# Optimization experiments

Hardware: AMD Instinct MI355X
Metric: run time of the kernel (lower is better)

## Reference

```python
import jax, jax.numpy as jnp
import numpy as np

EPS_LOG = 1e-8
EPS_CHECK = 1e-4


def to_float8(x, exp_bits=4, mant_bits=3):
    # fp8 emulation: sign/abs/log2/floor/clamp/round chain
    max_exp = 2 ** (exp_bits - 1) - 1
    min_exp = -max_exp
    scale = 2.0 ** mant_bits
    sign = jnp.sign(x)
    x_abs = jnp.abs(x)
    exp = jnp.clip(jnp.floor(jnp.log2(x_abs + EPS_LOG)), min_exp, max_exp)
    pow2 = jnp.exp2(exp)
    mant = x_abs / pow2 - 1.0
    mant_q = jnp.round(mant * scale) / scale
    return sign * (1.0 + mant_q) * pow2


def checksum_verify(left, right, epsilon=EPS_CHECK):
    # ABFT: augment left with a column-sum row, right with a row-sum column
    left_cs = jnp.concatenate([left, jnp.sum(left, axis=0, keepdims=True)], axis=0)
    right_cs = jnp.concatenate([right, jnp.sum(right, axis=1, keepdims=True)], axis=1)
    prod_cs = left_cs @ right_cs  # [(m+1), (n+1)]
    output = prod_cs[:-1, :-1]
    row_sum_check = prod_cs[:-1, -1]
    col_sum_check = prod_cs[-1, :-1]
    col_diff = jnp.abs(jnp.sum(output, axis=0) - col_sum_check)
    row_diff = jnp.abs(jnp.sum(output, axis=1) - row_sum_check)
    mask = (row_diff > epsilon)[:, None] & (col_diff > epsilon)[None, :]
    return output, mask


def setup_inputs() -> dict:
    key = jax.random.key(0)
    kx, ku, kA, kB, kC = jax.random.split(key, 5)
    batch, n, m, p = 4096, 2048, 1024, 1024
    return {
        "x": jax.random.normal(kx, (batch, n), dtype=jnp.float32),
        "u": jax.random.normal(ku, (batch, m), dtype=jnp.float32),
        "A": jax.random.normal(kA, (n, n), dtype=jnp.float32),
        "B": jax.random.normal(kB, (n, m), dtype=jnp.float32),
        "C": jax.random.normal(kC, (p, n), dtype=jnp.float32),
    }


def reference(x, u, A, B, C):
    int_bits, frac_bits = 4, 3
    Aq = to_float8(A, int_bits, frac_bits)
    Bq = to_float8(B, int_bits, frac_bits)
    left_term, left_mask = checksum_verify(x, Aq.T)
    right_term, right_mask = checksum_verify(u, Bq.T)
    x_next = to_float8(left_term + right_term, int_bits, frac_bits)
    _ = left_mask | right_mask  # mask computed but discarded in forward (as in torch)
    Cq = to_float8(C, int_bits, frac_bits)
    y = to_float8(x_next @ Cq.T, int_bits, frac_bits)
    return (x_next, y)
```

## Files before the change

kernel.cpp:

```cpp
#include <hip/hip_runtime.h>
#include <hip/hip_bf16.h>
#include <stdint.h>

typedef __bf16 bf16_t;
typedef __attribute__((ext_vector_type(8))) __bf16 bf16x8;
typedef __attribute__((ext_vector_type(4))) float f32x4;

__device__ __forceinline__ float q8(float v) {
    float a = __builtin_fabsf(v);
    float z = a + 1e-8f;
    int ei = ((__float_as_int(z) >> 23) & 0xff) - 127;
    ei = ei > 7 ? 7 : (ei < -7 ? -7 : ei);
    float p  = __int_as_float((ei + 127) << 23);
    float ip = __int_as_float((127 - ei) << 23);
    float m  = __builtin_fmaf(a, ip, -1.0f);
    float mq = __builtin_rintf(m * 8.0f) * 0.125f;
    float r  = (1.0f + mq) * p;
    return v < 0.0f ? -r : r;
}

__device__ __forceinline__ void gload_lds16(const bf16_t* g, bf16_t* l) {
    __builtin_amdgcn_global_load_lds(
        (__attribute__((address_space(1))) void*)(g),
        (__attribute__((address_space(3))) void*)(l), 16, 0, 0);
}

__device__ __forceinline__ bf16x8 cvt8(float4 a, float4 b) {
    bf16x8 o = { (bf16_t)a.x, (bf16_t)a.y, (bf16_t)a.z, (bf16_t)a.w,
                 (bf16_t)b.x, (bf16_t)b.y, (bf16_t)b.z, (bf16_t)b.w };
    return o;
}
__device__ __forceinline__ bf16x8 q8x8(float4 a, float4 b) {
    bf16x8 o = { (bf16_t)q8(a.x), (bf16_t)q8(a.y), (bf16_t)q8(a.z), (bf16_t)q8(a.w),
                 (bf16_t)q8(b.x), (bf16_t)q8(b.y), (bf16_t)q8(b.z), (bf16_t)q8(b.w) };
    return o;
}

__global__ void pack_all(const float* __restrict__ x, const float* __restrict__ u,
                         const float* __restrict__ A, const float* __restrict__ B,
                         const float* __restrict__ C,
                         bf16_t* __restrict__ XU, bf16_t* __restrict__ AB,
                         bf16_t* __restrict__ CQ) {
    const unsigned bid = blockIdx.x;
    const int tid = threadIdx.x;
    if (bid < 4096u) {
        size_t r = bid; int col = tid * 8;
        float4 v0 = *(const float4*)&x[r * 2048 + col];
        float4 v1 = *(const float4*)&x[r * 2048 + col + 4];
        *(bf16x8*)&XU[r * 3072 + col] = cvt8(v0, v1);
    } else if (bid < 6144u) {
        unsigned b = bid - 4096u;
        size_t r = b * 2 + (tid >> 7); int col = (tid & 127) * 8;
        float4 v0 = *(const float4*)&u[r * 1024 + col];
        float4 v1 = *(const float4*)&u[r * 1024 + col + 4];
        *(bf16x8*)&XU[r * 3072 + 2048 + col] = cvt8(v0, v1);
    } else if (bid < 8192u) {
        size_t r = bid - 6144u; int col = tid * 8;
        float4 v0 = *(const float4*)&A[r * 2048 + col];
        float4 v1 = *(const float4*)&A[r * 2048 + col + 4];
        *(bf16x8*)&AB[r * 3072 + col] = q8x8(v0, v1);
    } else if (bid < 9216u) {
        unsigned b = bid - 8192u;
        size_t r = b * 2 + (tid >> 7); int col = (tid & 127) * 8;
        float4 v0 = *(const float4*)&B[r * 1024 + col];
        float4 v1 = *(const float4*)&B[r * 1024 + col + 4];
        *(bf16x8*)&AB[r * 3072 + 2048 + col] = q8x8(v0, v1);
    } else {
        size_t r = bid - 9216u; int col = tid * 8;
        float4 v0 = *(const float4*)&C[r * 2048 + col];
        float4 v1 = *(const float4*)&C[r * 2048 + col + 4];
        *(bf16x8*)&CQ[r * 2048 + col] = q8x8(v0, v1);
    }
}

template<int NBX, bool DUAL>
__global__ __launch_bounds__(512, 4)
void gemm_q8_kernel(const bf16_t* __restrict__ A, const bf16_t* __restrict__ B,
                    float* __restrict__ outf, bf16_t* __restrict__ outb,
                    int M, int N, int K) {
    constexpr int BM = 128;
    constexpr int BN = 128;
    constexpr int BK = 64;
    constexpr int PX = NBX / 2;

    __shared__ alignas(16) bf16_t sA[2][BM * BK];
    __shared__ alignas(16) bf16_t sB[2][BN * BK];

    const int tid  = threadIdx.x;
    const int lane = tid & 63;
    const int wave = tid >> 6;
    const int wm   = wave & 3;
    const int wn   = wave >> 2;
    const int ln16 = lane & 15;
    const int quad = lane >> 4;

    const int b   = blockIdx.x;
    const int xcd = b & 7;
    const int g   = b >> 3;
    const int bx  = (xcd & 1) * PX + (g % PX);
    const int by  = (xcd >> 1) * 8 + (g / PX);
    const int brow = by * BM;
    const int bcol = bx * BN;

    const bf16_t* gA[2];
    const bf16_t* gB[2];
#pragma unroll
    for (int it = 0; it < 2; ++it) {
        int L = it * 512 + tid;
        int r = L >> 3, c = L & 7;
        gA[it] = A + (size_t)(brow + r) * K + (c ^ (r & 7)) * 8;
        gB[it] = B + (size_t)(bcol + r) * K + (c ^ (r & 7)) * 8;
    }

    int a_off[2][2], b_off[4][2];
#pragma unroll
    for (int im = 0; im < 2; ++im) {
        int r = wm * 32 + im * 16 + ln16;
#pragma unroll
        for (int s = 0; s < 2; ++s) {
            int cg = s * 4 + quad;
            a_off[im][s] = (r * 8 + (cg ^ (r & 7))) * 8;
        }
    }
#pragma unroll
    for (int in = 0; in < 4; ++in) {
        int r = wn * 64 + in * 16 + ln16;
#pragma unroll
        for (int s = 0; s < 2; ++s) {
            int cg = s * 4 + quad;
            b_off[in][s] = (r * 8 + (cg ^ (r & 7))) * 8;
        }
    }

    f32x4 acc[2][4];
#pragma unroll
    for (int im = 0; im < 2; ++im)
#pragma unroll
        for (int in = 0; in < 4; ++in)
            acc[im][in] = (f32x4){0.f, 0.f, 0.f, 0.f};

    auto stage_tile = [&](int cur) {
#pragma unroll
        for (int it = 0; it < 2; ++it) {
            gload_lds16(gA[it], &sA[cur][(it * 512 + wave * 64) * 8]);
            gA[it] += BK;
        }
#pragma unroll
        for (int it = 0; it < 2; ++it) {
            gload_lds16(gB[it], &sB[cur][(it * 512 + wave * 64) * 8]);
            gB[it] += BK;
        }
    };

    auto compute_tile = [&](int cur) {
        const bf16_t* bA = sA[cur];
        const bf16_t* bB = sB[cur];
        __builtin_amdgcn_s_setprio(1);
#pragma unroll
        for (int s = 0; s < 2; ++s) {
            bf16x8 af[2], bfv[4];
#pragma unroll
            for (int im = 0; im < 2; ++im) af[im]  = *(const bf16x8*)(bA + a_off[im][s]);
#pragma unroll
            for (int in = 0; in < 4; ++in) bfv[in] = *(const bf16x8*)(bB + b_off[in][s]);
#pragma unroll
            for (int im = 0; im < 2; ++im)
#pragma unroll
                for (int in = 0; in < 4; ++in)
                    acc[im][in] = __builtin_amdgcn_mfma_f32_16x16x32_bf16(
                        af[im], bfv[in], acc[im][in], 0, 0, 0);
        }
        __builtin_amdgcn_s_setprio(0);
    };

    stage_tile(0);
    stage_tile(1);

    const int NT = K / BK;
    for (int t = 0; t < NT - 1; ++t) {
        const int cur = t & 1;
        asm volatile("s_waitcnt vmcnt(4)" ::: "memory");
        __builtin_amdgcn_s_barrier();
        asm volatile("" ::: "memory");
        compute_tile(cur);
        asm volatile("" ::: "memory");
        __builtin_amdgcn_s_barrier();
        if (t + 2 < NT) stage_tile(cur);
    }
    asm volatile("s_waitcnt vmcnt(0)" ::: "memory");
    __builtin_amdgcn_s_barrier();
    asm volatile("" ::: "memory");
    compute_tile((NT - 1) & 1);

    const int rbase = quad * 4;
#pragma unroll
    for (int im = 0; im < 2; ++im) {
#pragma unroll
        for (int in = 0; in < 4; ++in) {
            int gm = brow + wm * 32 + im * 16 + rbase;
            int gn = bcol + wn * 64 + in * 16 + ln16;
#pragma unroll
            for (int r = 0; r < 4; ++r) {
                float v = q8(acc[im][in][r]);
                outf[(size_t)(gm + r) * N + gn] = v;
                if (DUAL) outb[(size_t)(gm + r) * N + gn] = (bf16_t)v;
            }
        }
    }
}

extern "C" void kernel_launch(void* const* d_in, const int* in_sizes, int n_in,
                              void* d_out, int out_size, void* d_ws, size_t ws_size,
                              hipStream_t stream) {
    const float* x = (const float*)d_in[0];
    const float* u = (const float*)d_in[1];
    const float* A = (const float*)d_in[2];
    const float* B = (const float*)d_in[3];
    const float* C = (const float*)d_in[4];

    float* outf = (float*)d_out;
    float* xnf  = outf;
    float* yf   = outf + (size_t)4096 * 2048;

    uint8_t* ws = (uint8_t*)d_ws;
    bf16_t* XU = (bf16_t*)ws;
    bf16_t* AB = (bf16_t*)(ws + (size_t)25165824);
    bf16_t* CQ = (bf16_t*)(ws + (size_t)25165824 + 12582912);
    bf16_t* XN = (bf16_t*)(ws + (size_t)25165824 + 12582912 + 4194304);

    pack_all<<<dim3(10240), 256, 0, stream>>>(x, u, A, B, C, XU, AB, CQ);

    gemm_q8_kernel<16, true><<<dim3(512), 512, 0, stream>>>(
        XU, AB, xnf, XN, 4096, 2048, 3072);
    gemm_q8_kernel<8, false><<<dim3(256), 512, 0, stream>>>(
        XN, CQ, yf, nullptr, 4096, 1024, 2048);
}
```

Measured before the change: 212.0 us.

## Rewrite GEMM as 8-phase pipelined kernel with 256-row tiles

```diff
diff --git a/kernel.cpp b/kernel.cpp
--- a/kernel.cpp
+++ b/kernel.cpp
@@ -23,6 +23,13 @@
     __builtin_amdgcn_global_load_lds(
         (__attribute__((address_space(1))) void*)(g),
         (__attribute__((address_space(3))) void*)(l), 16, 0, 0);
+}
+
+template<int N> __device__ __forceinline__ void vmwait() {
+    if constexpr (N == 0)      asm volatile("s_waitcnt vmcnt(0)" ::: "memory");
+    else if constexpr (N == 5) asm volatile("s_waitcnt vmcnt(5)" ::: "memory");
+    else if constexpr (N == 6) asm volatile("s_waitcnt vmcnt(6)" ::: "memory");
+    else if constexpr (N == 8) asm volatile("s_waitcnt vmcnt(8)" ::: "memory");
 }
 
 __device__ __forceinline__ bf16x8 cvt8(float4 a, float4 b) {
@@ -73,18 +80,36 @@
     }
 }
 
-template<int NBX, bool DUAL>
-__global__ __launch_bounds__(512, 4)
-void gemm_q8_kernel(const bf16_t* __restrict__ A, const bf16_t* __restrict__ B,
-                    float* __restrict__ outf, bf16_t* __restrict__ outb,
-                    int M, int N, int K) {
-    constexpr int BM = 128;
-    constexpr int BN = 128;
+#define PHASE_CORE(i0, i1)                                                     \
+    __builtin_amdgcn_s_barrier();                                              \
+    asm volatile("s_waitcnt lgkmcnt(0)" ::: "memory");                         \
+    __builtin_amdgcn_s_setprio(1);                                             \
+    _Pragma("unroll")                                                          \
+    for (int in = 0; in < NI; ++in)                                            \
+        acc[i0][in] = __builtin_amdgcn_mfma_f32_16x16x32_bf16(af0, bfv[in],    \
+                                                              acc[i0][in], 0, 0, 0); \
+    _Pragma("unroll")                                                          \
+    for (int in = 0; in < NI; ++in)                                            \
+        acc[i1][in] = __builtin_amdgcn_mfma_f32_16x16x32_bf16(af1, bfv[in],    \
+                                                              acc[i1][in], 0, 0, 0); \
+    __builtin_amdgcn_s_setprio(0);
+
+template<int BN, bool DUAL>
+__global__ __launch_bounds__(512, 2)
+void gemm_q8_8ph(const bf16_t* __restrict__ Ap, const bf16_t* __restrict__ Bp,
+                 float* __restrict__ outf, bf16_t* __restrict__ outb,
+                 int N, int K) {
+    constexpr int BM = 256;
     constexpr int BK = 64;
-    constexpr int PX = NBX / 2;
-
-    __shared__ alignas(16) bf16_t sA[2][BM * BK];
-    __shared__ alignas(16) bf16_t sB[2][BN * BK];
+    constexpr int NI = BN / 32;
+    constexpr int BL = BN / 64;
+    constexpr int VM_MID = 4 + 2 * BL;
+    constexpr int VM_END = 4 + BL;
+    constexpr int ASLOT = BM * 32;
+    constexpr int BBUF  = BN * 64;
+
+    __shared__ alignas(16) bf16_t sAr[4][ASLOT];
+    __shared__ alignas(16) bf16_t sBr[3][BBUF];
 
     const int tid  = threadIdx.x;
     const int lane = tid & 63;
@@ -97,34 +122,42 @@
     const int b   = blockIdx.x;
     const int xcd = b & 7;
     const int g   = b >> 3;
-    const int bx  = (xcd & 1) * PX + (g % PX);
-    const int by  = (xcd >> 1) * 8 + (g / PX);
+    const int bx  = (xcd & 1) * 8 + (g & 7);
+    const int by  = (xcd >> 1) * 4 + (g >> 3);
     const int brow = by * BM;
     const int bcol = bx * BN;
 
-    const bf16_t* gA[2];
-    const bf16_t* gB[2];
-#pragma unroll
-    for (int it = 0; it < 2; ++it) {
-        int L = it * 512 + tid;
-        int r = L >> 3, c = L & 7;
-        gA[it] = A + (size_t)(brow + r) * K + (c ^ (r & 7)) * 8;
-        gB[it] = B + (size_t)(bcol + r) * K + (c ^ (r & 7)) * 8;
-    }
-
-    int a_off[2][2], b_off[4][2];
-#pragma unroll
-    for (int im = 0; im < 2; ++im) {
-        int r = wm * 32 + im * 16 + ln16;
-#pragma unroll
-        for (int s = 0; s < 2; ++s) {
-            int cg = s * 4 + quad;
-            a_off[im][s] = (r * 8 + (cg ^ (r & 7))) * 8;
-        }
-    }
-#pragma unroll
-    for (int in = 0; in < 4; ++in) {
-        int r = wn * 64 + in * 16 + ln16;
+    const bf16_t *pA0a, *pA0b, *pA1a, *pA1b;
+    {
+        int L0 = tid,       r0 = L0 >> 2, c0 = L0 & 3;
+        int L1 = 512 + tid, r1 = L1 >> 2, c1 = L1 & 3;
+        size_t ro0 = (size_t)(brow + r0) * K;
+        size_t ro1 = (size_t)(brow + r1) * K;
+        int cs0 = (c0 ^ ((r0 >> 1) & 3)) * 8;
+        int cs1 = (c1 ^ ((r1 >> 1) & 3)) * 8;
+        pA0a = Ap + ro0 + cs0;        pA0b = Ap + ro1 + cs1;
+        pA1a = Ap + ro0 + 32 + cs0;   pA1b = Ap + ro1 + 32 + cs1;
+    }
+    const bf16_t *pB0, *pB1 = nullptr;
+    {
+        int L = tid, r = L >> 3, c = L & 7;
+        pB0 = Bp + (size_t)(bcol + r) * K + (c ^ (r & 7)) * 8;
+    }
+    if constexpr (BL == 2) {
+        int L = 512 + tid, r = L >> 3, c = L & 7;
+        pB1 = Bp + (size_t)(bcol + r) * K + (c ^ (r & 7)) * 8;
+    }
+
+    int a_off[4];
+#pragma unroll
+    for (int im = 0; im < 4; ++im) {
+        int r = wm * 64 + im * 16 + ln16;
+        a_off[im] = (r * 4 + (quad ^ ((r >> 1) & 3))) * 8;
+    }
+    int b_off[NI][2];
+#pragma unroll
+    for (int in = 0; in < NI; ++in) {
+        int r = wn * (BN / 2) + in * 16 + ln16;
 #pragma unroll
         for (int s = 0; s < 2; ++s) {
             int cg = s * 4 + quad;
@@ -132,73 +165,92 @@
         }
     }
 
-    f32x4 acc[2][4];
-#pragma unroll
-    for (int im = 0; im < 2; ++im)
-#pragma unroll
-        for (int in = 0; in < 4; ++in)
+    f32x4 acc[4][NI];
+#pragma unroll
+    for (int im = 0; im < 4; ++im)
+#pragma unroll
+        for (int in = 0; in < NI; ++in)
             acc[im][in] = (f32x4){0.f, 0.f, 0.f, 0.f};
 
-    auto stage_tile = [&](int cur) {
-#pragma unroll
-        for (int it = 0; it < 2; ++it) {
-            gload_lds16(gA[it], &sA[cur][(it * 512 + wave * 64) * 8]);
-            gA[it] += BK;
-        }
-#pragma unroll
-        for (int it = 0; it < 2; ++it) {
-            gload_lds16(gB[it], &sB[cur][(it * 512 + wave * 64) * 8]);
-            gB[it] += BK;
-        }
-    };
-
-    auto compute_tile = [&](int cur) {
-        const bf16_t* bA = sA[cur];
-        const bf16_t* bB = sB[cur];
-        __builtin_amdgcn_s_setprio(1);
-#pragma unroll
-        for (int s = 0; s < 2; ++s) {
-            bf16x8 af[2], bfv[4];
-#pragma unroll
-            for (int im = 0; im < 2; ++im) af[im]  = *(const bf16x8*)(bA + a_off[im][s]);
-#pragma unroll
-            for (int in = 0; in < 4; ++in) bfv[in] = *(const bf16x8*)(bB + b_off[in][s]);
-#pragma unroll
-            for (int im = 0; im < 2; ++im)
-#pragma unroll
-                for (int in = 0; in < 4; ++in)
-                    acc[im][in] = __builtin_amdgcn_mfma_f32_16x16x32_bf16(
-                        af[im], bfv[in], acc[im][in], 0, 0, 0);
-        }
-        __builtin_amdgcn_s_setprio(0);
-    };
-
-    stage_tile(0);
-    stage_tile(1);
-
-    const int NT = K / BK;
-    for (int t = 0; t < NT - 1; ++t) {
-        const int cur = t & 1;
-        asm volatile("s_waitcnt vmcnt(4)" ::: "memory");
-        __builtin_amdgcn_s_barrier();
-        asm volatile("" ::: "memory");
-        compute_tile(cur);
-        asm volatile("" ::: "memory");
-        __builtin_amdgcn_s_barrier();
-        if (t + 2 < NT) stage_tile(cur);
-    }
-    asm volatile("s_waitcnt vmcnt(0)" ::: "memory");
+    gload_lds16(pA0a, &sAr[0][wave * 512]);        pA0a += BK;
+    gload_lds16(pA0b, &sAr[0][4096 + wave * 512]); pA0b += BK;
+    gload_lds16(pA1a, &sAr[1][wave * 512]);        pA1a += BK;
+    gload_lds16(pA1b, &sAr[1][4096 + wave * 512]); pA1b += BK;
+    gload_lds16(pA0a, &sAr[2][wave * 512]);        pA0a += BK;
+    gload_lds16(pA0b, &sAr[2][4096 + wave * 512]); pA0b += BK;
+    gload_lds16(pB0, &sBr[0][wave * 512]);         pB0 += BK;
+    if constexpr (BL == 2) { gload_lds16(pB1, &sBr[0][4096 + wave * 512]); pB1 += BK; }
+    gload_lds16(pB0, &sBr[1][wave * 512]);         pB0 += BK;
+    if constexpr (BL == 2) { gload_lds16(pB1, &sBr[1][4096 + wave * 512]); pB1 += BK; }
+    vmwait<0>();
     __builtin_amdgcn_s_barrier();
     asm volatile("" ::: "memory");
-    compute_tile((NT - 1) & 1);
+
+    const int NT = K / BK;
+    int bb = 0;
+    for (int t = 0; t < NT; ++t) {
+        const int sl0 = (t & 1) << 1;
+        const int sl1 = sl0 | 1;
+        const bool strong = (t < 2) | (t >= NT - 2);
+
+        bf16x8 af0, af1, bfv[NI];
+
+        af0 = *(const bf16x8*)&sAr[sl0][a_off[0]];
+        af1 = *(const bf16x8*)&sAr[sl0][a_off[1]];
+#pragma unroll
+        for (int in = 0; in < NI; ++in)
+            bfv[in] = *(const bf16x8*)&sBr[bb][b_off[in][0]];
+        if (t + 1 < NT) {
+            const int sa = (sl0 + 3) & 3;
+            gload_lds16(pA1a, &sAr[sa][wave * 512]);        pA1a += BK;
+            gload_lds16(pA1b, &sAr[sa][4096 + wave * 512]); pA1b += BK;
+        }
+        PHASE_CORE(0, 1)
+        __builtin_amdgcn_s_barrier();
+        asm volatile("" ::: "memory");
+
+        af0 = *(const bf16x8*)&sAr[sl0][a_off[2]];
+        af1 = *(const bf16x8*)&sAr[sl0][a_off[3]];
+        if (t + 2 < NT) {
+            const int bs = (bb + 2 >= 3) ? bb - 1 : bb + 2;
+            gload_lds16(pB0, &sBr[bs][wave * 512]);         pB0 += BK;
+            if constexpr (BL == 2) { gload_lds16(pB1, &sBr[bs][4096 + wave * 512]); pB1 += BK; }
+        }
+        PHASE_CORE(2, 3)
+        if (strong) vmwait<0>(); else vmwait<VM_MID>();
+        __builtin_amdgcn_s_barrier();
+        asm volatile("" ::: "memory");
+
+        af0 = *(const bf16x8*)&sAr[sl1][a_off[0]];
+        af1 = *(const bf16x8*)&sAr[sl1][a_off[1]];
+#pragma unroll
+        for (int in = 0; in < NI; ++in)
+            bfv[in] = *(const bf16x8*)&sBr[bb][b_off[in][1]];
+        if (t + 2 < NT) {
+            gload_lds16(pA0a, &sAr[sl0][wave * 512]);        pA0a += BK;
+            gload_lds16(pA0b, &sAr[sl0][4096 + wave * 512]); pA0b += BK;
+        }
+        PHASE_CORE(0, 1)
+        __builtin_amdgcn_s_barrier();
+        asm volatile("" ::: "memory");
+
+        af0 = *(const bf16x8*)&sAr[sl1][a_off[2]];
+        af1 = *(const bf16x8*)&sAr[sl1][a_off[3]];
+        PHASE_CORE(2, 3)
+        if (strong) vmwait<0>(); else vmwait<VM_END>();
+        __builtin_amdgcn_s_barrier();
+        asm volatile("" ::: "memory");
+
+        bb = (bb == 2) ? 0 : bb + 1;
+    }
 
     const int rbase = quad * 4;
 #pragma unroll
-    for (int im = 0; im < 2; ++im) {
-#pragma unroll
-        for (int in = 0; in < 4; ++in) {
-            int gm = brow + wm * 32 + im * 16 + rbase;
-            int gn = bcol + wn * 64 + in * 16 + ln16;
+    for (int im = 0; im < 4; ++im) {
+#pragma unroll
+        for (int in = 0; in < NI; ++in) {
+            int gm = brow + wm * 64 + im * 16 + rbase;
+            int gn = bcol + wn * (BN / 2) + in * 16 + ln16;
 #pragma unroll
             for (int r = 0; r < 4; ++r) {
                 float v = q8(acc[im][in][r]);
@@ -230,8 +282,8 @@
 
     pack_all<<<dim3(10240), 256, 0, stream>>>(x, u, A, B, C, XU, AB, CQ);
 
-    gemm_q8_kernel<16, true><<<dim3(512), 512, 0, stream>>>(
-        XU, AB, xnf, XN, 4096, 2048, 3072);
-    gemm_q8_kernel<8, false><<<dim3(256), 512, 0, stream>>>(
-        XN, CQ, yf, nullptr, 4096, 1024, 2048);
-}
+    gemm_q8_8ph<128, true><<<dim3(256), 512, 0, stream>>>(
+        XU, AB, xnf, XN, 2048, 3072);
+    gemm_q8_8ph<64, false><<<dim3(256), 512, 0, stream>>>(
+        XN, CQ, yf, nullptr, 1024, 2048);
+}
```

Result: slower. 229.1 us (+8.1%).

## Use 256-row tiles with triple-buffered LDS and one barrier per K step

Applied to the files above, without the earlier changes.

```diff
diff --git a/kernel.cpp b/kernel.cpp
--- a/kernel.cpp
+++ b/kernel.cpp
@@ -23,6 +23,12 @@
     __builtin_amdgcn_global_load_lds(
         (__attribute__((address_space(1))) void*)(g),
         (__attribute__((address_space(3))) void*)(l), 16, 0, 0);
+}
+
+template<int N> __device__ __forceinline__ void vmwait() {
+    if constexpr (N == 0)      asm volatile("s_waitcnt vmcnt(0)" ::: "memory");
+    else if constexpr (N == 5) asm volatile("s_waitcnt vmcnt(5)" ::: "memory");
+    else if constexpr (N == 6) asm volatile("s_waitcnt vmcnt(6)" ::: "memory");
 }
 
 __device__ __forceinline__ bf16x8 cvt8(float4 a, float4 b) {
@@ -73,18 +79,21 @@
     }
 }
 
-template<int NBX, bool DUAL>
-__global__ __launch_bounds__(512, 4)
-void gemm_q8_kernel(const bf16_t* __restrict__ A, const bf16_t* __restrict__ B,
-                    float* __restrict__ outf, bf16_t* __restrict__ outb,
-                    int M, int N, int K) {
-    constexpr int BM = 128;
-    constexpr int BN = 128;
+template<int BN, bool DUAL>
+__global__ __launch_bounds__(512, 2)
+void gemm_q8_r3(const bf16_t* __restrict__ Ap, const bf16_t* __restrict__ Bp,
+                float* __restrict__ outf, bf16_t* __restrict__ outb,
+                int N, int K) {
+    constexpr int BM = 256;
     constexpr int BK = 64;
-    constexpr int PX = NBX / 2;
-
-    __shared__ alignas(16) bf16_t sA[2][BM * BK];
-    __shared__ alignas(16) bf16_t sB[2][BN * BK];
+    constexpr int NI    = BN / 32;
+    constexpr int B_ITS = BN / 64;
+    constexpr int TOT   = 4 + B_ITS;
+    constexpr int ABUF  = BM * BK;
+    constexpr int BBUF  = BN * BK;
+
+    __shared__ alignas(16) bf16_t sA[3][ABUF];
+    __shared__ alignas(16) bf16_t sB[3][BBUF];
 
     const int tid  = threadIdx.x;
     const int lane = tid & 63;
@@ -97,25 +106,30 @@
     const int b   = blockIdx.x;
     const int xcd = b & 7;
     const int g   = b >> 3;
-    const int bx  = (xcd & 1) * PX + (g % PX);
-    const int by  = (xcd >> 1) * 8 + (g / PX);
+    const int bx  = (xcd & 1) * 8 + (g & 7);
+    const int by  = (xcd >> 1) * 4 + (g >> 3);
     const int brow = by * BM;
     const int bcol = bx * BN;
 
-    const bf16_t* gA[2];
-    const bf16_t* gB[2];
-#pragma unroll
-    for (int it = 0; it < 2; ++it) {
+    const bf16_t* gA[4];
+#pragma unroll
+    for (int it = 0; it < 4; ++it) {
         int L = it * 512 + tid;
         int r = L >> 3, c = L & 7;
-        gA[it] = A + (size_t)(brow + r) * K + (c ^ (r & 7)) * 8;
-        gB[it] = B + (size_t)(bcol + r) * K + (c ^ (r & 7)) * 8;
-    }
-
-    int a_off[2][2], b_off[4][2];
-#pragma unroll
-    for (int im = 0; im < 2; ++im) {
-        int r = wm * 32 + im * 16 + ln16;
+        gA[it] = Ap + (size_t)(brow + r) * K + (c ^ (r & 7)) * 8;
+    }
+    const bf16_t* gB[B_ITS];
+#pragma unroll
+    for (int it = 0; it < B_ITS; ++it) {
+        int L = it * 512 + tid;
+        int r = L >> 3, c = L & 7;
+        gB[it] = Bp + (size_t)(bcol + r) * K + (c ^ (r & 7)) * 8;
+    }
+
+    int a_off[4][2], b_off[NI][2];
+#pragma unroll
+    for (int im = 0; im < 4; ++im) {
+        int r = wm * 64 + im * 16 + ln16;
 #pragma unroll
         for (int s = 0; s < 2; ++s) {
             int cg = s * 4 + quad;
@@ -123,8 +137,8 @@
         }
     }
 #pragma unroll
-    for (int in = 0; in < 4; ++in) {
-        int r = wn * 64 + in * 16 + ln16;
+    for (int in = 0; in < NI; ++in) {
+        int r = wn * (BN / 2) + in * 16 + ln16;
 #pragma unroll
         for (int s = 0; s < 2; ++s) {
             int cg = s * 4 + quad;
@@ -132,73 +146,84 @@
         }
     }
 
-    f32x4 acc[2][4];
-#pragma unroll
-    for (int im = 0; im < 2; ++im)
-#pragma unroll
-        for (int in = 0; in < 4; ++in)
+    f32x4 acc[4][NI];
+#pragma unroll
+    for (int im = 0; im < 4; ++im)
+#pragma unroll
+        for (int in = 0; in < NI; ++in)
             acc[im][in] = (f32x4){0.f, 0.f, 0.f, 0.f};
 
-    auto stage_tile = [&](int cur) {
-#pragma unroll
-        for (int it = 0; it < 2; ++it) {
-            gload_lds16(gA[it], &sA[cur][(it * 512 + wave * 64) * 8]);
+    auto STAGE = [&](int sb) {
+#pragma unroll
+        for (int it = 0; it < 4; ++it) {
+            gload_lds16(gA[it], &sA[sb][(it * 512 + wave * 64) * 8]);
             gA[it] += BK;
         }
 #pragma unroll
-        for (int it = 0; it < 2; ++it) {
-            gload_lds16(gB[it], &sB[cur][(it * 512 + wave * 64) * 8]);
+        for (int it = 0; it < B_ITS; ++it) {
+            gload_lds16(gB[it], &sB[sb][(it * 512 + wave * 64) * 8]);
             gB[it] += BK;
         }
     };
 
-    auto compute_tile = [&](int cur) {
-        const bf16_t* bA = sA[cur];
-        const bf16_t* bB = sB[cur];
-        __builtin_amdgcn_s_setprio(1);
-#pragma unroll
-        for (int s = 0; s < 2; ++s) {
-            bf16x8 af[2], bfv[4];
-#pragma unroll
-            for (int im = 0; im < 2; ++im) af[im]  = *(const bf16x8*)(bA + a_off[im][s]);
-#pragma unroll
-            for (int in = 0; in < 4; ++in) bfv[in] = *(const bf16x8*)(bB + b_off[in][s]);
-#pragma unroll
-            for (int im = 0; im < 2; ++im)
-#pragma unroll
-                for (int in = 0; in < 4; ++in)
+    STAGE(0);
+    STAGE(1);
+    vmwait<TOT>();
+    __builtin_amdgcn_s_barrier();
+    asm volatile("" ::: "memory");
+
+    const int NT = K / BK;
+    int rb = 0;
+    for (int t = 0; t < NT; ++t) {
+        if (t + 2 < NT) {
+            int sb = rb + 2; if (sb >= 3) sb -= 3;
+            STAGE(sb);
+        }
+        const bf16_t* bA = sA[rb];
+        const bf16_t* bB = sB[rb];
+        {
+            bf16x8 af[4], bfv[NI];
+#pragma unroll
+            for (int im = 0; im < 4; ++im) af[im]  = *(const bf16x8*)(bA + a_off[im][0]);
+#pragma unroll
+            for (int in = 0; in < NI; ++in) bfv[in] = *(const bf16x8*)(bB + b_off[in][0]);
+            __builtin_amdgcn_s_setprio(1);
+#pragma unroll
+            for (int im = 0; im < 4; ++im)
+#pragma unroll
+                for (int in = 0; in < NI; ++in)
                     acc[im][in] = __builtin_amdgcn_mfma_f32_16x16x32_bf16(
                         af[im], bfv[in], acc[im][in], 0, 0, 0);
-        }
-        __builtin_amdgcn_s_setprio(0);
-    };
-
-    stage_tile(0);
-    stage_tile(1);
-
-    const int NT = K / BK;
-    for (int t = 0; t < NT - 1; ++t) {
-        const int cur = t & 1;
-        asm volatile("s_waitcnt vmcnt(4)" ::: "memory");
+            __builtin_amdgcn_s_setprio(0);
+        }
+        {
+            bf16x8 af[4], bfv[NI];
+#pragma unroll
+            for (int im = 0; im < 4; ++im) af[im]  = *(const bf16x8*)(bA + a_off[im][1]);
+#pragma unroll
+            for (int in = 0; in < NI; ++in) bfv[in] = *(const bf16x8*)(bB + b_off[in][1]);
+            __builtin_amdgcn_s_setprio(1);
+#pragma unroll
+            for (int im = 0; im < 4; ++im)
+#pragma unroll
+                for (int in = 0; in < NI; ++in)
+                    acc[im][in] = __builtin_amdgcn_mfma_f32_16x16x32_bf16(
+                        af[im], bfv[in], acc[im][in], 0, 0, 0);
+            __builtin_amdgcn_s_setprio(0);
+        }
+        if (t + 2 < NT) vmwait<TOT>(); else vmwait<0>();
         __builtin_amdgcn_s_barrier();
         asm volatile("" ::: "memory");
-        compute_tile(cur);
-        asm volatile("" ::: "memory");
-        __builtin_amdgcn_s_barrier();
-        if (t + 2 < NT) stage_tile(cur);
-    }
-    asm volatile("s_waitcnt vmcnt(0)" ::: "memory");
-    __builtin_amdgcn_s_barrier();
-    asm volatile("" ::: "memory");
-    compute_tile((NT - 1) & 1);
+        rb = rb + 1; if (rb == 3) rb = 0;
+    }
 
     const int rbase = quad * 4;
 #pragma unroll
-    for (int im = 0; im < 2; ++im) {
-#pragma unroll
-        for (int in = 0; in < 4; ++in) {
-            int gm = brow + wm * 32 + im * 16 + rbase;
-            int gn = bcol + wn * 64 + in * 16 + ln16;
+    for (int im = 0; im < 4; ++im) {
+#pragma unroll
+        for (int in = 0; in < NI; ++in) {
+            int gm = brow + wm * 64 + im * 16 + rbase;
+            int gn = bcol + wn * (BN / 2) + in * 16 + ln16;
 #pragma unroll
             for (int r = 0; r < 4; ++r) {
                 float v = q8(acc[im][in][r]);
@@ -230,8 +255,8 @@
 
     pack_all<<<dim3(10240), 256, 0, stream>>>(x, u, A, B, C, XU, AB, CQ);
 
-    gemm_q8_kernel<16, true><<<dim3(512), 512, 0, stream>>>(
-        XU, AB, xnf, XN, 4096, 2048, 3072);
-    gemm_q8_kernel<8, false><<<dim3(256), 512, 0, stream>>>(
-        XN, CQ, yf, nullptr, 4096, 1024, 2048);
-}
+    gemm_q8_r3<128, true><<<dim3(256), 512, 0, stream>>>(
+        XU, AB, xnf, XN, 2048, 3072);
+    gemm_q8_r3<64, false><<<dim3(256), 512, 0, stream>>>(
+        XN, CQ, yf, nullptr, 1024, 2048);
+}
```

Measured after the change: 230.9 us. +8.9%, slower.
